# Performance work log

Hardware: AMD Instinct MI355X
Metric: run time of the kernel (lower is better)

The kernel has to match this reference:

```python
import jax, jax.numpy as jnp
import numpy as np

INITIAL_RADIUS = 1.0


def setup_inputs() -> dict:
    key = jax.random.key(0)
    k1, k2, k3 = jax.random.split(key, 3)
    B, N, S = 4, 8192, 2048
    xyz = jax.random.normal(k1, (B, 3, N), dtype=jnp.float32)
    sparse_xyz = jax.random.normal(k2, (B, 3, S), dtype=jnp.float32)
    sparse_flow = jax.random.normal(k3, (B, 3, S), dtype=jnp.float32)
    return {"xyz": xyz, "sparse_xyz": sparse_xyz, "sparse_flow": sparse_flow,
            "resol_factor": 1}


def reference(xyz, sparse_xyz, sparse_flow, resol_factor):
    # xyz: [B,3,N], sparse_xyz/sparse_flow: [B,3,S]
    radius = INITIAL_RADIUS * resol_factor
    x = jnp.transpose(xyz, (0, 2, 1))          # [B,N,3] dense query points
    y = jnp.transpose(sparse_xyz, (0, 2, 1))   # [B,S,3] sparse support points
    f = jnp.transpose(sparse_flow, (0, 2, 1))  # [B,S,3] sparse flow values
    B, S, _ = y.shape
    w = jnp.ones((B, S, 1), dtype=x.dtype)     # uniform sample weights

    # squared pairwise distances D2[b,n,s] = ||x_bn - y_bs||^2
    x2 = jnp.sum(x * x, axis=-1, keepdims=True)            # [B,N,1]
    y2 = jnp.sum(y * y, axis=-1)[:, None, :]               # [B,1,S]
    xy = jnp.einsum('bnd,bsd->bns', x, y)                  # [B,N,S]
    d2 = x2 + y2 - 2.0 * xy

    # Gaussian Nadaraya-Watson kernel weights
    k = jnp.exp(-d2 / (radius * radius))                   # [B,N,S]

    num = jnp.einsum('bns,bsd->bnd', k, f * w)             # [B,N,3]
    den = jnp.einsum('bns,bsd->bnd', k, w)                 # [B,N,1]
    dense = num / den                                      # [B,N,3]
    return jnp.transpose(dense, (0, 2, 1))                 # [B,3,N]
```

## Files before the change

### kernel.cpp

```cpp
#include <hip/hip_runtime.h>


constexpr int B_ = 4, N_ = 8192, S_ = 2048;
constexpr int BLOCK = 256, PPT = 8;
constexpr int PTS_PER_BLOCK = BLOCK * PPT;
constexpr int NBPB = N_ / PTS_PER_BLOCK;
constexpr int NB = B_ * NBPB;
constexpr int BN = B_ * N_;
constexpr float LOG2E = 1.4426950408889634f;

template <int CHUNK>
__global__ __launch_bounds__(BLOCK, 4) void uf2_main(
    const float* __restrict__ xyz,
    const float* __restrict__ sxyz,
    const float* __restrict__ sflow,
    const int* __restrict__ resol,
    float4* __restrict__ part)
{
    __shared__ float4 As[CHUNK];
    __shared__ float4 Fs[CHUNK];

    const int nb = blockIdx.x % NB;
    const int sc = blockIdx.x / NB;
    const int b  = nb / NBPB;
    const int n0 = (nb % NBPB) * PTS_PER_BLOCK;
    const int s0 = sc * CHUNK;

    const float r = (float)resol[0];
    const float inv_r2 = 1.0f / (r * r);
    const float c2 = 2.0f * inv_r2 * LOG2E;
    const float cy = -inv_r2 * LOG2E;

    const float* yb = sxyz  + b * 3 * S_;
    const float* fb = sflow + b * 3 * S_;
    for (int t = threadIdx.x; t < CHUNK; t += BLOCK) {
        const int s = s0 + t;
        const float yx = yb[s], yy = yb[S_ + s], yz = yb[2 * S_ + s];
        const float fx = fb[s], fy = fb[S_ + s], fz = fb[2 * S_ + s];
        As[t] = make_float4(c2 * yx, c2 * yy, c2 * yz,
                            cy * (yx * yx + yy * yy + yz * yz));
        Fs[t] = make_float4(fx, fy, fz, 0.0f);
    }
    __syncthreads();

    const float* xb = xyz + b * 3 * N_;
    float px[PPT], py[PPT], pz[PPT];
    float ax[PPT], ay[PPT], az[PPT], aw[PPT];
#pragma unroll
    for (int p = 0; p < PPT; ++p) {
        const int n = n0 + threadIdx.x + p * BLOCK;
        px[p] = xb[n]; py[p] = xb[N_ + n]; pz[p] = xb[2 * N_ + n];
        ax[p] = 0.f; ay[p] = 0.f; az[p] = 0.f; aw[p] = 0.f;
    }

#pragma unroll 2
    for (int t = 0; t < CHUNK; ++t) {
        const float4 a = As[t];
        const float4 f = Fs[t];
#pragma unroll
        for (int p = 0; p < PPT; ++p) {
            float e = fmaf(pz[p], a.z, a.w);
            e = fmaf(py[p], a.y, e);
            e = fmaf(px[p], a.x, e);
            const float k = __builtin_amdgcn_exp2f(e);
            ax[p] = fmaf(k, f.x, ax[p]);
            ay[p] = fmaf(k, f.y, ay[p]);
            az[p] = fmaf(k, f.z, az[p]);
            aw[p] += k;
        }
    }

#pragma unroll
    for (int p = 0; p < PPT; ++p) {
        const int g = b * N_ + n0 + threadIdx.x + p * BLOCK;
        part[(size_t)sc * BN + g] = make_float4(ax[p], ay[p], az[p], aw[p]);
    }
}

__global__ __launch_bounds__(BLOCK) void uf2_combine(
    const float4* __restrict__ part, float* __restrict__ out, int SC)
{
    const int g = blockIdx.x * BLOCK + threadIdx.x;
    float4 s0 = make_float4(0.f, 0.f, 0.f, 0.f);
    float4 s1 = s0, s2 = s0, s3 = s0;
    int c = 0;
    for (; c + 4 <= SC; c += 4) {
        const float4 p0 = part[(size_t)(c + 0) * BN + g];
        const float4 p1 = part[(size_t)(c + 1) * BN + g];
        const float4 p2 = part[(size_t)(c + 2) * BN + g];
        const float4 p3 = part[(size_t)(c + 3) * BN + g];
        s0.x += p0.x; s0.y += p0.y; s0.z += p0.z; s0.w += p0.w;
        s1.x += p1.x; s1.y += p1.y; s1.z += p1.z; s1.w += p1.w;
        s2.x += p2.x; s2.y += p2.y; s2.z += p2.z; s2.w += p2.w;
        s3.x += p3.x; s3.y += p3.y; s3.z += p3.z; s3.w += p3.w;
    }
    for (; c < SC; ++c) {
        const float4 p = part[(size_t)c * BN + g];
        s0.x += p.x; s0.y += p.y; s0.z += p.z; s0.w += p.w;
    }
    const float sx = (s0.x + s1.x) + (s2.x + s3.x);
    const float sy = (s0.y + s1.y) + (s2.y + s3.y);
    const float sz = (s0.z + s1.z) + (s2.z + s3.z);
    const float sw = (s0.w + s1.w) + (s2.w + s3.w);
    const float inv = 1.0f / sw;
    const int b = g >> 13;
    const int n = g & (N_ - 1);
    float* ob = out + b * 3 * N_;
    ob[n]          = sx * inv;
    ob[N_ + n]     = sy * inv;
    ob[2 * N_ + n] = sz * inv;
}

__global__ __launch_bounds__(BLOCK, 1) void uf2_fused(
    const float* __restrict__ xyz,
    const float* __restrict__ sxyz,
    const float* __restrict__ sflow,
    const int* __restrict__ resol,
    float* __restrict__ out)
{
    constexpr int FPPT = 4;
    constexpr int PTS = BLOCK * FPPT;
    __shared__ float4 As[S_];
    __shared__ float4 Fs[S_];

    const int nb = blockIdx.x;
    const int b  = nb / (N_ / PTS);
    const int n0 = (nb % (N_ / PTS)) * PTS;

    const float r = (float)resol[0];
    const float inv_r2 = 1.0f / (r * r);
    const float c2 = 2.0f * inv_r2 * LOG2E;
    const float cy = -inv_r2 * LOG2E;

    const float* yb = sxyz  + b * 3 * S_;
    const float* fb = sflow + b * 3 * S_;
    for (int t = threadIdx.x; t < S_; t += BLOCK) {
        const float yx = yb[t], yy = yb[S_ + t], yz = yb[2 * S_ + t];
        const float fx = fb[t], fy = fb[S_ + t], fz = fb[2 * S_ + t];
        As[t] = make_float4(c2 * yx, c2 * yy, c2 * yz,
                            cy * (yx * yx + yy * yy + yz * yz));
        Fs[t] = make_float4(fx, fy, fz, 0.0f);
    }
    __syncthreads();

    const float* xb = xyz + b * 3 * N_;
    float px[FPPT], py[FPPT], pz[FPPT];
    float4 acc[FPPT];
#pragma unroll
    for (int p = 0; p < FPPT; ++p) {
        const int n = n0 + threadIdx.x + p * BLOCK;
        px[p] = xb[n]; py[p] = xb[N_ + n]; pz[p] = xb[2 * N_ + n];
        acc[p] = make_float4(0.f, 0.f, 0.f, 0.f);
    }
#pragma unroll 4
    for (int t = 0; t < S_; ++t) {
        const float4 a = As[t];
        const float4 f = Fs[t];
#pragma unroll
        for (int p = 0; p < FPPT; ++p) {
            float e = fmaf(pz[p], a.z, a.w);
            e = fmaf(py[p], a.y, e);
            e = fmaf(px[p], a.x, e);
            const float k = __builtin_amdgcn_exp2f(e);
            acc[p].x = fmaf(k, f.x, acc[p].x);
            acc[p].y = fmaf(k, f.y, acc[p].y);
            acc[p].z = fmaf(k, f.z, acc[p].z);
            acc[p].w += k;
        }
    }
#pragma unroll
    for (int p = 0; p < FPPT; ++p) {
        const int n = n0 + threadIdx.x + p * BLOCK;
        const float inv = 1.0f / acc[p].w;
        float* ob = out + b * 3 * N_;
        ob[n]          = acc[p].x * inv;
        ob[N_ + n]     = acc[p].y * inv;
        ob[2 * N_ + n] = acc[p].z * inv;
    }
}

extern "C" void kernel_launch(void* const* d_in, const int* in_sizes, int n_in,
                              void* d_out, int out_size, void* d_ws, size_t ws_size,
                              hipStream_t stream)
{
    const float* xyz   = (const float*)d_in[0];
    const float* sxyz  = (const float*)d_in[1];
    const float* sflow = (const float*)d_in[2];
    const int*   resol = (const int*)d_in[3];
    float* out = (float*)d_out;
    float4* part = (float4*)d_ws;

    const size_t per_chunk = (size_t)BN * sizeof(float4);
    int SC = 16;
    while (SC > 1 && (size_t)SC * per_chunk > ws_size) SC >>= 1;

    if ((size_t)SC * per_chunk > ws_size) {
        uf2_fused<<<dim3(BN / 1024), dim3(BLOCK), 0, stream>>>(
            xyz, sxyz, sflow, resol, out);
        return;
    }

    dim3 grid(NB * SC), blk(BLOCK);
    switch (SC) {
        case 16: uf2_main<S_ / 16><<<grid, blk, 0, stream>>>(xyz, sxyz, sflow, resol, part); break;
        case 8:  uf2_main<S_ / 8 ><<<grid, blk, 0, stream>>>(xyz, sxyz, sflow, resol, part); break;
        case 4:  uf2_main<S_ / 4 ><<<grid, blk, 0, stream>>>(xyz, sxyz, sflow, resol, part); break;
        case 2:  uf2_main<S_ / 2 ><<<grid, blk, 0, stream>>>(xyz, sxyz, sflow, resol, part); break;
        default: uf2_main<S_     ><<<grid, blk, 0, stream>>>(xyz, sxyz, sflow, resol, part); break;
    }
    uf2_combine<<<dim3(BN / BLOCK), dim3(BLOCK), 0, stream>>>(part, out, SC);
}
```

Measured before the change: 31.25 us.

## Use packed FP32 FMA for distance and accumulation, halve points per thread

Rewrites the inner loop so pairs of query points are processed with v_pk_fma_f32 / v_pk_add_f32 via inline asm, with shared-memory support data stored duplicated so each pair shares the same operand. Points per thread drop from 8 to 4 and the S split rises from 16 to 32 chunks, which keeps the grid filled. The aim is to roughly halve VALU instruction count for the FMA work, leaving exp2 as the scalar bottleneck. The cost is more LDS reads per iteration and twice as many partial sums for the combine kernel to read.

```diff
diff --git a/kernel.cpp b/kernel.cpp
--- a/kernel.cpp
+++ b/kernel.cpp
@@ -1,13 +1,22 @@
 #include <hip/hip_runtime.h>
 
 
+typedef float v2f __attribute__((ext_vector_type(2)));
+
 constexpr int B_ = 4, N_ = 8192, S_ = 2048;
-constexpr int BLOCK = 256, PPT = 8;
+constexpr int BLOCK = 256, PPT = 4, NQ = PPT / 2;
 constexpr int PTS_PER_BLOCK = BLOCK * PPT;
 constexpr int NBPB = N_ / PTS_PER_BLOCK;
 constexpr int NB = B_ * NBPB;
 constexpr int BN = B_ * N_;
 constexpr float LOG2E = 1.4426950408889634f;
+
+#define PK_FMA(d, a, b, c) \
+    asm("v_pk_fma_f32 %0, %1, %2, %3" : "=v"(d) : "v"(a), "v"(b), "v"(c))
+#define PK_FMA_ACC(acc, a, b) \
+    asm("v_pk_fma_f32 %0, %1, %2, %0" : "+v"(acc) : "v"(a), "v"(b))
+#define PK_ADD_ACC(acc, a) \
+    asm("v_pk_add_f32 %0, %1, %0" : "+v"(acc) : "v"(a))
 
 template <int CHUNK>
 __global__ __launch_bounds__(BLOCK, 4) void uf2_main(
@@ -17,8 +26,10 @@
     const int* __restrict__ resol,
     float4* __restrict__ part)
 {
-    __shared__ float4 As[CHUNK];
-    __shared__ float4 Fs[CHUNK];
+    __shared__ float4 A1[CHUNK];
+    __shared__ float4 A2[CHUNK];
+    __shared__ float4 F1[CHUNK];
+    __shared__ v2f    F2[CHUNK];
 
     const int nb = blockIdx.x % NB;
     const int sc = blockIdx.x / NB;
@@ -37,43 +48,61 @@
         const int s = s0 + t;
         const float yx = yb[s], yy = yb[S_ + s], yz = yb[2 * S_ + s];
         const float fx = fb[s], fy = fb[S_ + s], fz = fb[2 * S_ + s];
-        As[t] = make_float4(c2 * yx, c2 * yy, c2 * yz,
-                            cy * (yx * yx + yy * yy + yz * yz));
-        Fs[t] = make_float4(fx, fy, fz, 0.0f);
+        const float ax = c2 * yx, ay = c2 * yy, az = c2 * yz;
+        const float bias = cy * (yx * yx + yy * yy + yz * yz);
+        A1[t] = make_float4(ax, ax, ay, ay);
+        A2[t] = make_float4(az, az, bias, bias);
+        F1[t] = make_float4(fx, fx, fy, fy);
+        F2[t] = (v2f){fz, fz};
     }
     __syncthreads();
 
     const float* xb = xyz + b * 3 * N_;
-    float px[PPT], py[PPT], pz[PPT];
-    float ax[PPT], ay[PPT], az[PPT], aw[PPT];
-#pragma unroll
-    for (int p = 0; p < PPT; ++p) {
-        const int n = n0 + threadIdx.x + p * BLOCK;
-        px[p] = xb[n]; py[p] = xb[N_ + n]; pz[p] = xb[2 * N_ + n];
-        ax[p] = 0.f; ay[p] = 0.f; az[p] = 0.f; aw[p] = 0.f;
+    v2f px2[NQ], py2[NQ], pz2[NQ];
+    v2f acx[NQ], acy[NQ], acz[NQ], acw[NQ];
+#pragma unroll
+    for (int q = 0; q < NQ; ++q) {
+        const int na = n0 + threadIdx.x + (2 * q) * BLOCK;
+        const int nc = na + BLOCK;
+        px2[q] = (v2f){xb[na], xb[nc]};
+        py2[q] = (v2f){xb[N_ + na], xb[N_ + nc]};
+        pz2[q] = (v2f){xb[2 * N_ + na], xb[2 * N_ + nc]};
+        acx[q] = (v2f){0.f, 0.f}; acy[q] = (v2f){0.f, 0.f};
+        acz[q] = (v2f){0.f, 0.f}; acw[q] = (v2f){0.f, 0.f};
     }
 
 #pragma unroll 2
     for (int t = 0; t < CHUNK; ++t) {
-        const float4 a = As[t];
-        const float4 f = Fs[t];
-#pragma unroll
-        for (int p = 0; p < PPT; ++p) {
-            float e = fmaf(pz[p], a.z, a.w);
-            e = fmaf(py[p], a.y, e);
-            e = fmaf(px[p], a.x, e);
-            const float k = __builtin_amdgcn_exp2f(e);
-            ax[p] = fmaf(k, f.x, ax[p]);
-            ay[p] = fmaf(k, f.y, ay[p]);
-            az[p] = fmaf(k, f.z, az[p]);
-            aw[p] += k;
+        const float4 a1 = A1[t];
+        const float4 a2 = A2[t];
+        const float4 f1 = F1[t];
+        const v2f    fz2 = F2[t];
+        const v2f ax2 = (v2f){a1.x, a1.y}, ay2 = (v2f){a1.z, a1.w};
+        const v2f az2 = (v2f){a2.x, a2.y}, bi2 = (v2f){a2.z, a2.w};
+        const v2f fx2 = (v2f){f1.x, f1.y}, fy2 = (v2f){f1.z, f1.w};
+#pragma unroll
+        for (int q = 0; q < NQ; ++q) {
+            v2f e2;
+            PK_FMA(e2, pz2[q], az2, bi2);
+            PK_FMA_ACC(e2, py2[q], ay2);
+            PK_FMA_ACC(e2, px2[q], ax2);
+            v2f k2;
+            k2.x = __builtin_amdgcn_exp2f(e2.x);
+            k2.y = __builtin_amdgcn_exp2f(e2.y);
+            PK_FMA_ACC(acx[q], k2, fx2);
+            PK_FMA_ACC(acy[q], k2, fy2);
+            PK_FMA_ACC(acz[q], k2, fz2);
+            PK_ADD_ACC(acw[q], k2);
         }
     }
 
 #pragma unroll
-    for (int p = 0; p < PPT; ++p) {
-        const int g = b * N_ + n0 + threadIdx.x + p * BLOCK;
-        part[(size_t)sc * BN + g] = make_float4(ax[p], ay[p], az[p], aw[p]);
+    for (int q = 0; q < NQ; ++q) {
+        const int ga = b * N_ + n0 + threadIdx.x + (2 * q) * BLOCK;
+        part[(size_t)sc * BN + ga] =
+            make_float4(acx[q].x, acy[q].x, acz[q].x, acw[q].x);
+        part[(size_t)sc * BN + ga + BLOCK] =
+            make_float4(acx[q].y, acy[q].y, acz[q].y, acw[q].y);
     }
 }
 
@@ -191,7 +220,7 @@
     float4* part = (float4*)d_ws;
 
     const size_t per_chunk = (size_t)BN * sizeof(float4);
-    int SC = 16;
+    int SC = 32;
     while (SC > 1 && (size_t)SC * per_chunk > ws_size) SC >>= 1;
 
     if ((size_t)SC * per_chunk > ws_size) {
@@ -202,6 +231,7 @@
 
     dim3 grid(NB * SC), blk(BLOCK);
     switch (SC) {
+        case 32: uf2_main<S_ / 32><<<grid, blk, 0, stream>>>(xyz, sxyz, sflow, resol, part); break;
         case 16: uf2_main<S_ / 16><<<grid, blk, 0, stream>>>(xyz, sxyz, sflow, resol, part); break;
         case 8:  uf2_main<S_ / 8 ><<<grid, blk, 0, stream>>>(xyz, sxyz, sflow, resol, part); break;
         case 4:  uf2_main<S_ / 4 ><<<grid, blk, 0, stream>>>(xyz, sxyz, sflow, resol, part); break;
```

Result: no change. 31.70 us (+1.4%).

## Fuse split-S combine into main kernel via last-block atomic counter

Applied to the files above, without the earlier changes.

Drops the separate combine kernel. Each split-S block now bumps a per-tile atomic counter after writing its partials, and the last block to arrive reduces all partials and writes the normalized output. A hipMemsetAsync clears the counters before each launch. This removes one kernel launch and its serialization at the cost of a memset, threadfences and a tail reduction done by only some blocks. The launch bound also drops from 4 to 2 waves per SIMD.

```diff
diff --git a/kernel.cpp b/kernel.cpp
--- a/kernel.cpp
+++ b/kernel.cpp
@@ -2,20 +2,22 @@
 
 
 constexpr int B_ = 4, N_ = 8192, S_ = 2048;
-constexpr int BLOCK = 256, PPT = 8;
+constexpr int BLOCK = 256, PPT = 8, SC = 16;
 constexpr int PTS_PER_BLOCK = BLOCK * PPT;
 constexpr int NBPB = N_ / PTS_PER_BLOCK;
 constexpr int NB = B_ * NBPB;
+constexpr int CHUNK = S_ / SC;
 constexpr int BN = B_ * N_;
 constexpr float LOG2E = 1.4426950408889634f;
 
-template <int CHUNK>
-__global__ __launch_bounds__(BLOCK, 4) void uf2_main(
+__global__ __launch_bounds__(BLOCK, 2) void uf2_one(
     const float* __restrict__ xyz,
     const float* __restrict__ sxyz,
     const float* __restrict__ sflow,
     const int* __restrict__ resol,
-    float4* __restrict__ part)
+    float4* __restrict__ part,
+    int* __restrict__ cnt,
+    float* __restrict__ out)
 {
     __shared__ float4 As[CHUNK];
     __shared__ float4 Fs[CHUNK];
@@ -75,40 +77,45 @@
         const int g = b * N_ + n0 + threadIdx.x + p * BLOCK;
         part[(size_t)sc * BN + g] = make_float4(ax[p], ay[p], az[p], aw[p]);
     }
-}
-
-__global__ __launch_bounds__(BLOCK) void uf2_combine(
-    const float4* __restrict__ part, float* __restrict__ out, int SC)
-{
-    const int g = blockIdx.x * BLOCK + threadIdx.x;
-    float4 s0 = make_float4(0.f, 0.f, 0.f, 0.f);
-    float4 s1 = s0, s2 = s0, s3 = s0;
-    int c = 0;
-    for (; c + 4 <= SC; c += 4) {
-        const float4 p0 = part[(size_t)(c + 0) * BN + g];
-        const float4 p1 = part[(size_t)(c + 1) * BN + g];
-        const float4 p2 = part[(size_t)(c + 2) * BN + g];
-        const float4 p3 = part[(size_t)(c + 3) * BN + g];
-        s0.x += p0.x; s0.y += p0.y; s0.z += p0.z; s0.w += p0.w;
-        s1.x += p1.x; s1.y += p1.y; s1.z += p1.z; s1.w += p1.w;
-        s2.x += p2.x; s2.y += p2.y; s2.z += p2.z; s2.w += p2.w;
-        s3.x += p3.x; s3.y += p3.y; s3.z += p3.z; s3.w += p3.w;
-    }
-    for (; c < SC; ++c) {
-        const float4 p = part[(size_t)c * BN + g];
-        s0.x += p.x; s0.y += p.y; s0.z += p.z; s0.w += p.w;
-    }
-    const float sx = (s0.x + s1.x) + (s2.x + s3.x);
-    const float sy = (s0.y + s1.y) + (s2.y + s3.y);
-    const float sz = (s0.z + s1.z) + (s2.z + s3.z);
-    const float sw = (s0.w + s1.w) + (s2.w + s3.w);
-    const float inv = 1.0f / sw;
-    const int b = g >> 13;
-    const int n = g & (N_ - 1);
-    float* ob = out + b * 3 * N_;
-    ob[n]          = sx * inv;
-    ob[N_ + n]     = sy * inv;
-    ob[2 * N_ + n] = sz * inv;
+
+    __threadfence();
+    __syncthreads();
+    __shared__ int is_last;
+    if (threadIdx.x == 0) {
+        const int old = atomicAdd(&cnt[nb], 1);
+        is_last = (old == SC - 1);
+    }
+    __syncthreads();
+    if (!is_last) return;
+
+    __threadfence();
+#pragma unroll
+    for (int p = 0; p < PPT; ++p) {
+        const int g = b * N_ + n0 + threadIdx.x + p * BLOCK;
+        float4 s0v = make_float4(0.f, 0.f, 0.f, 0.f);
+        float4 s1v = s0v, s2v = s0v, s3v = s0v;
+#pragma unroll
+        for (int c = 0; c < SC; c += 4) {
+            const float4 p0 = part[(size_t)(c + 0) * BN + g];
+            const float4 p1 = part[(size_t)(c + 1) * BN + g];
+            const float4 p2 = part[(size_t)(c + 2) * BN + g];
+            const float4 p3 = part[(size_t)(c + 3) * BN + g];
+            s0v.x += p0.x; s0v.y += p0.y; s0v.z += p0.z; s0v.w += p0.w;
+            s1v.x += p1.x; s1v.y += p1.y; s1v.z += p1.z; s1v.w += p1.w;
+            s2v.x += p2.x; s2v.y += p2.y; s2v.z += p2.z; s2v.w += p2.w;
+            s3v.x += p3.x; s3v.y += p3.y; s3v.z += p3.z; s3v.w += p3.w;
+        }
+        const float sx = (s0v.x + s1v.x) + (s2v.x + s3v.x);
+        const float sy = (s0v.y + s1v.y) + (s2v.y + s3v.y);
+        const float sz = (s0v.z + s1v.z) + (s2v.z + s3v.z);
+        const float sw = (s0v.w + s1v.w) + (s2v.w + s3v.w);
+        const float inv = 1.0f / sw;
+        const int n = n0 + threadIdx.x + p * BLOCK;
+        float* ob = out + b * 3 * N_;
+        ob[n]          = sx * inv;
+        ob[N_ + n]     = sy * inv;
+        ob[2 * N_ + n] = sz * inv;
+    }
 }
 
 __global__ __launch_bounds__(BLOCK, 1) void uf2_fused(
@@ -188,25 +195,21 @@
     const float* sflow = (const float*)d_in[2];
     const int*   resol = (const int*)d_in[3];
     float* out = (float*)d_out;
-    float4* part = (float4*)d_ws;
-
-    const size_t per_chunk = (size_t)BN * sizeof(float4);
-    int SC = 16;
-    while (SC > 1 && (size_t)SC * per_chunk > ws_size) SC >>= 1;
-
-    if ((size_t)SC * per_chunk > ws_size) {
+
+    const size_t part_bytes = (size_t)SC * BN * sizeof(float4);
+    const size_t need = part_bytes + NB * sizeof(int);
+
+    if (need > ws_size) {
         uf2_fused<<<dim3(BN / 1024), dim3(BLOCK), 0, stream>>>(
             xyz, sxyz, sflow, resol, out);
         return;
     }
 
-    dim3 grid(NB * SC), blk(BLOCK);
-    switch (SC) {
-        case 16: uf2_main<S_ / 16><<<grid, blk, 0, stream>>>(xyz, sxyz, sflow, resol, part); break;
-        case 8:  uf2_main<S_ / 8 ><<<grid, blk, 0, stream>>>(xyz, sxyz, sflow, resol, part); break;
-        case 4:  uf2_main<S_ / 4 ><<<grid, blk, 0, stream>>>(xyz, sxyz, sflow, resol, part); break;
-        case 2:  uf2_main<S_ / 2 ><<<grid, blk, 0, stream>>>(xyz, sxyz, sflow, resol, part); break;
-        default: uf2_main<S_     ><<<grid, blk, 0, stream>>>(xyz, sxyz, sflow, resol, part); break;
-    }
-    uf2_combine<<<dim3(BN / BLOCK), dim3(BLOCK), 0, stream>>>(part, out, SC);
+    float4* part = (float4*)d_ws;
+    int*    cnt  = (int*)((char*)d_ws + part_bytes);
+
+    hipMemsetAsync(cnt, 0, NB * sizeof(int), stream);
+
+    uf2_one<<<dim3(NB * SC), dim3(BLOCK), 0, stream>>>(
+        xyz, sxyz, sflow, resol, part, cnt, out);
 }
```

Result: slower. 64.78 us (+107.3%).
